# Kernel optimization log

Hardware: AMD Instinct MI355X
Metric: run time of the kernel (lower is better)

The kernel has to match this reference:

```python
import jax, jax.numpy as jnp
import numpy as np

N_NODES = 100000
N_EDGES = 1600000
IN_F, HID_F, OUT_F = 128, 64, 40


def setup_inputs() -> dict:
    key = jax.random.key(0)
    ks = jax.random.split(key, 12)
    features = jax.random.normal(ks[0], (N_NODES, IN_F), jnp.float32)
    src = jax.random.randint(ks[1], (N_EDGES,), 0, N_NODES, jnp.int32)
    dst = jax.random.randint(ks[2], (N_EDGES,), 0, N_NODES, jnp.int32)

    def glorot(k, fi, fo):
        s = np.sqrt(6.0 / (fi + fo)).astype(np.float32)
        return jax.random.uniform(k, (fi, fo), jnp.float32, -s, s)

    return {
        "features": features, "src": src, "dst": dst,
        "W0": glorot(ks[3], IN_F, HID_F), "b0": jnp.zeros((HID_F,), jnp.float32),
        "W1": glorot(ks[4], HID_F, HID_F), "b1": jnp.zeros((HID_F,), jnp.float32),
        "W2": glorot(ks[5], HID_F, HID_F), "b2": jnp.zeros((HID_F,), jnp.float32),
        "W3": glorot(ks[6], HID_F, OUT_F), "b3": jnp.zeros((OUT_F,), jnp.float32),
    }


def _degree_norms(src, dst, n, dtype):
    ones = jnp.ones(src.shape[0], dtype)
    out_deg = jax.ops.segment_sum(ones, src, num_segments=n)
    in_deg = jax.ops.segment_sum(ones, dst, num_segments=n)
    # norm='both': D_src^{-1/2} on sources, D_dst^{-1/2} on destinations (0 for isolated nodes)
    ns = jnp.where(out_deg > 0, jax.lax.rsqrt(jnp.maximum(out_deg, 1.0)), 0.0)[:, None]
    nd = jnp.where(in_deg > 0, jax.lax.rsqrt(jnp.maximum(in_deg, 1.0)), 0.0)[:, None]
    return ns, nd


def _graph_conv(x, W, b, src, dst, ns, nd, relu):
    # transform first (in_feats >= out_feats here), then aggregate: traffic-optimal order
    h = (x * ns) @ W                                   # [N, out_f]
    agg = jax.ops.segment_sum(h[src], dst, num_segments=x.shape[0])  # SpMM gather/scatter
    out = agg * nd + b
    return jax.nn.relu(out) if relu else out


def reference(features, src, dst, W0, b0, W1, b1, W2, b2, W3, b3):
    ns, nd = _degree_norms(src, dst, features.shape[0], features.dtype)
    h = _graph_conv(features, W0, b0, src, dst, ns, nd, True)
    h = _graph_conv(h, W1, b1, src, dst, ns, nd, True)   # dropout = identity (eval)
    h = _graph_conv(h, W2, b2, src, dst, ns, nd, True)
    h = _graph_conv(h, W3, b3, src, dst, ns, nd, False)
    return h
```

## Files before the change

### kernel.cpp

```cpp
#include <hip/hip_runtime.h>
#include <hip/hip_fp16.h>


constexpr int BLK = 256;
constexpr int BIN_SHIFT = 7;
constexpr int BIN_NODES = 128;
constexpr int BIN_CAP = 3072;
constexpr int MAX_NB = 800;
constexpr int EPT = 8;

__global__ void zero_int(int* p, int n) {
  int i = blockIdx.x * blockDim.x + threadIdx.x;
  if (i < n) p[i] = 0;
}

__global__ __launch_bounds__(BLK) void binfill(const int* __restrict__ src,
                                               const int* __restrict__ dst,
                                               int* __restrict__ deg_out,
                                               int* __restrict__ bin_cnt,
                                               int* __restrict__ codes,
                                               int e, int nb) {
  __shared__ int hist[MAX_NB];
  __shared__ int basec[MAX_NB];
  const int tid = threadIdx.x;
  for (int i = tid; i < nb; i += BLK) hist[i] = 0;
  __syncthreads();

  const int B0 = blockIdx.x * (BLK * EPT);
  int s[EPT], d[EPT];
  #pragma unroll
  for (int c = 0; c < EPT / 4; ++c) {
    int i = B0 + (c * BLK + tid) * 4;
    if (i + 3 < e) {
      int4 sv = *(const int4*)(src + i);
      int4 dv = *(const int4*)(dst + i);
      s[4 * c + 0] = sv.x; s[4 * c + 1] = sv.y;
      s[4 * c + 2] = sv.z; s[4 * c + 3] = sv.w;
      d[4 * c + 0] = dv.x; d[4 * c + 1] = dv.y;
      d[4 * c + 2] = dv.z; d[4 * c + 3] = dv.w;
    } else {
      #pragma unroll
      for (int j = 0; j < 4; ++j) {
        int ii = i + j;
        if (ii < e) { s[4 * c + j] = src[ii]; d[4 * c + j] = dst[ii]; }
        else { s[4 * c + j] = 0; d[4 * c + j] = -1; }
      }
    }
  }

  #pragma unroll
  for (int j = 0; j < EPT; ++j) {
    if (d[j] >= 0) {
      atomicAdd(&deg_out[s[j]], 1);
      atomicAdd(&hist[d[j] >> BIN_SHIFT], 1);
    }
  }
  __syncthreads();
  for (int i = tid; i < nb; i += BLK) {
    int c = hist[i];
    basec[i] = c ? atomicAdd(&bin_cnt[i], c) : 0;
  }
  __syncthreads();
  #pragma unroll
  for (int j = 0; j < EPT; ++j) {
    if (d[j] >= 0) {
      int b = d[j] >> BIN_SHIFT;
      int ofs = atomicAdd(&basec[b], 1);
      if (ofs < BIN_CAP)
        codes[(size_t)b * BIN_CAP + ofs] = ((d[j] & (BIN_NODES - 1)) << 17) | s[j];
    }
  }
}

__global__ void norms_ns(const int* __restrict__ deg_out, float* ns, int n) {
  int i = blockIdx.x * blockDim.x + threadIdx.x;
  if (i < n) {
    int od = deg_out[i];
    ns[i] = od > 0 ? rsqrtf((float)od) : 0.f;
  }
}

__global__ __launch_bounds__(BLK) void scan_bins(const int* __restrict__ bin_cnt,
                                                 int* __restrict__ bin_base,
                                                 int* __restrict__ row_ptr,
                                                 int nb, int n) {
  const int tid = threadIdx.x;
  const int base = tid * 4;
  int v0 = 0, v1 = 0, v2 = 0, v3 = 0;
  if (base + 0 < nb) v0 = min(bin_cnt[base + 0], BIN_CAP);
  if (base + 1 < nb) v1 = min(bin_cnt[base + 1], BIN_CAP);
  if (base + 2 < nb) v2 = min(bin_cnt[base + 2], BIN_CAP);
  if (base + 3 < nb) v3 = min(bin_cnt[base + 3], BIN_CAP);
  int s = v0 + v1 + v2 + v3;
  const int lane = tid & 63, wid = tid >> 6;
  int incl = s;
  #pragma unroll
  for (int off = 1; off < 64; off <<= 1) {
    int t = __shfl_up(incl, off, 64);
    if (lane >= off) incl += t;
  }
  __shared__ int wtot[4];
  if (lane == 63) wtot[wid] = incl;
  __syncthreads();
  int woff = 0;
  for (int w = 0; w < wid; ++w) woff += wtot[w];
  int run = woff + (incl - s);
  if (base + 0 < nb) bin_base[base + 0] = run; run += v0;
  if (base + 1 < nb) bin_base[base + 1] = run; run += v1;
  if (base + 2 < nb) bin_base[base + 2] = run; run += v2;
  if (base + 3 < nb) bin_base[base + 3] = run; run += v3;
  if (tid == BLK - 1) {
    int total = wtot[0] + wtot[1] + wtot[2] + wtot[3];
    bin_base[nb] = total;
    row_ptr[n] = total;
  }
}

__global__ __launch_bounds__(BLK) void bin2csr(const int* __restrict__ codes,
                                               const int* __restrict__ bin_cnt,
                                               const int* __restrict__ bin_base,
                                               int* __restrict__ row_ptr,
                                               float* __restrict__ nd,
                                               int* __restrict__ esrc, int n) {
  __shared__ int scodes[BIN_CAP];
  __shared__ int hist[BIN_NODES];
  __shared__ int rowof[BIN_NODES];
  __shared__ int wsum[2];
  const int tid = threadIdx.x;
  const int bin = blockIdx.x;
  const int cnt = min(bin_cnt[bin], BIN_CAP);
  const int base = bin_base[bin];
  const int* cb = codes + (size_t)bin * BIN_CAP;

  if (tid < BIN_NODES) hist[tid] = 0;
  for (int i = tid; i < cnt; i += BLK) scodes[i] = cb[i];
  __syncthreads();
  for (int i = tid; i < cnt; i += BLK) atomicAdd(&hist[scodes[i] >> 17], 1);
  __syncthreads();

  if (tid < BIN_NODES) {
    int v = hist[tid];
    int incl = v;
    const int lane = tid & 63, wid = tid >> 6;
    #pragma unroll
    for (int off = 1; off < 64; off <<= 1) {
      int t = __shfl_up(incl, off, 64);
      if (lane >= off) incl += t;
    }
    if (lane == 63) wsum[wid] = incl;
    __syncthreads();
    int excl = incl - v + (wid ? wsum[0] : 0);
    rowof[tid] = excl;
    int node = bin * BIN_NODES + tid;
    if (node < n) {
      row_ptr[node] = base + excl;
      nd[node] = v > 0 ? rsqrtf((float)v) : 0.f;
    }
  } else {
    __syncthreads();
  }
  __syncthreads();

  for (int i = tid; i < cnt; i += BLK) {
    int code = scodes[i];
    int pos = atomicAdd(&rowof[code >> 17], 1);
    esrc[base + pos] = code & 0x1FFFF;
  }
}

template <int K, int F, int STRIDE>
__global__ __launch_bounds__(BLK) void gemm_tile(const float* __restrict__ x,
                                                 const float* __restrict__ W,
                                                 const float* __restrict__ ns,
                                                 __half* __restrict__ h, int n) {
  constexpr int KT = 64;
  constexpr int KP = KT + 4;
  __shared__ float sx[64 * KP];
  __shared__ float sW[KT * F];
  const int tid = threadIdx.x;
  const int n0 = blockIdx.x * 64;
  const int ft = tid & 15, nt = tid >> 4;
  const int fbase = (4 * ft < F) ? 4 * ft : 0;
  float acc[4][4] = {};

  for (int kt = 0; kt < K; kt += KT) {
    if (kt) __syncthreads();
    for (int i = tid; i < KT * F; i += BLK) sW[i] = W[kt * F + i];
    for (int idx = tid; idx < 64 * (KT / 4); idx += BLK) {
      int node = idx >> 4;
      int kk = idx & 15;
      int gn = min(n0 + node, n - 1);
      float4 v = *(const float4*)(x + (size_t)gn * K + kt + kk * 4);
      *(float4*)(sx + node * KP + kk * 4) = v;
    }
    __syncthreads();

    #pragma unroll 4
    for (int k0 = 0; k0 < KT; k0 += 4) {
      float4 xv0 = *(const float4*)(sx + (4 * nt + 0) * KP + k0);
      float4 xv1 = *(const float4*)(sx + (4 * nt + 1) * KP + k0);
      float4 xv2 = *(const float4*)(sx + (4 * nt + 2) * KP + k0);
      float4 xv3 = *(const float4*)(sx + (4 * nt + 3) * KP + k0);
      float4 w0 = *(const float4*)(sW + (k0 + 0) * F + fbase);
      float4 w1 = *(const float4*)(sW + (k0 + 1) * F + fbase);
      float4 w2 = *(const float4*)(sW + (k0 + 2) * F + fbase);
      float4 w3 = *(const float4*)(sW + (k0 + 3) * F + fbase);
#define GCN_STEP(C, WV)                                                  \
      acc[0][0] = fmaf(xv0.C, WV.x, acc[0][0]);                          \
      acc[0][1] = fmaf(xv0.C, WV.y, acc[0][1]);                          \
      acc[0][2] = fmaf(xv0.C, WV.z, acc[0][2]);                          \
      acc[0][3] = fmaf(xv0.C, WV.w, acc[0][3]);                          \
      acc[1][0] = fmaf(xv1.C, WV.x, acc[1][0]);                          \
      acc[1][1] = fmaf(xv1.C, WV.y, acc[1][1]);                          \
      acc[1][2] = fmaf(xv1.C, WV.z, acc[1][2]);                          \
      acc[1][3] = fmaf(xv1.C, WV.w, acc[1][3]);                          \
      acc[2][0] = fmaf(xv2.C, WV.x, acc[2][0]);                          \
      acc[2][1] = fmaf(xv2.C, WV.y, acc[2][1]);                          \
      acc[2][2] = fmaf(xv2.C, WV.z, acc[2][2]);                          \
      acc[2][3] = fmaf(xv2.C, WV.w, acc[2][3]);                          \
      acc[3][0] = fmaf(xv3.C, WV.x, acc[3][0]);                          \
      acc[3][1] = fmaf(xv3.C, WV.y, acc[3][1]);                          \
      acc[3][2] = fmaf(xv3.C, WV.z, acc[3][2]);                          \
      acc[3][3] = fmaf(xv3.C, WV.w, acc[3][3]);
      GCN_STEP(x, w0)
      GCN_STEP(y, w1)
      GCN_STEP(z, w2)
      GCN_STEP(w, w3)
#undef GCN_STEP
    }
  }

  #pragma unroll
  for (int i = 0; i < 4; ++i) {
    int node = n0 + 4 * nt + i;
    if (node < n && 4 * ft < F) {
      float s = ns[node];
      __half2 h0 = __floats2half2_rn(acc[i][0] * s, acc[i][1] * s);
      __half2 h1 = __floats2half2_rn(acc[i][2] * s, acc[i][3] * s);
      uint2 u;
      u.x = *(unsigned int*)&h0;
      u.y = *(unsigned int*)&h1;
      *(uint2*)(h + (size_t)node * STRIDE + 4 * ft) = u;
    }
  }
}

template <bool RELU>
__global__ void agg4h(const __half* __restrict__ h, const int* __restrict__ row_ptr,
                      const int* __restrict__ esrc, const float* __restrict__ nd,
                      const float* __restrict__ b, float* __restrict__ out, int n) {
  int tid = threadIdx.x;
  int node = blockIdx.x * 4 + (tid >> 6);
  if (node >= n) return;
  int lane = tid & 63;
  int g = lane >> 4;
  int fl = lane & 15;
  int beg = row_ptr[node], end = row_ptr[node + 1];
  float ax = 0.f, ay = 0.f, az = 0.f, aw = 0.f;
  #pragma unroll 4
  for (int k = beg + g; k < end; k += 4) {
    int s = esrc[k];
    uint2 u = *(const uint2*)(h + (size_t)s * 64 + fl * 4);
    float2 f0 = __half22float2(*(__half2*)&u.x);
    float2 f1 = __half22float2(*(__half2*)&u.y);
    ax += f0.x; ay += f0.y; az += f1.x; aw += f1.y;
  }
  ax += __shfl_xor(ax, 16, 64); ay += __shfl_xor(ay, 16, 64);
  az += __shfl_xor(az, 16, 64); aw += __shfl_xor(aw, 16, 64);
  ax += __shfl_xor(ax, 32, 64); ay += __shfl_xor(ay, 32, 64);
  az += __shfl_xor(az, 32, 64); aw += __shfl_xor(aw, 32, 64);
  if (lane < 16) {
    float ndv = nd[node];
    float4 bv = ((const float4*)b)[fl];
    float4 o;
    o.x = ax * ndv + bv.x;
    o.y = ay * ndv + bv.y;
    o.z = az * ndv + bv.z;
    o.w = aw * ndv + bv.w;
    if (RELU) {
      o.x = fmaxf(o.x, 0.f); o.y = fmaxf(o.y, 0.f);
      o.z = fmaxf(o.z, 0.f); o.w = fmaxf(o.w, 0.f);
    }
    *(float4*)(out + (size_t)node * 64 + fl * 4) = o;
  }
}

__global__ void agg40h(const __half* __restrict__ h, const int* __restrict__ row_ptr,
                       const int* __restrict__ esrc, const float* __restrict__ nd,
                       const float* __restrict__ b, float* __restrict__ out, int n) {
  int tid = threadIdx.x;
  int node = blockIdx.x * 4 + (tid >> 6);
  if (node >= n) return;
  int lane = tid & 63;
  int g = lane >> 4;
  int fl = lane & 15;
  int beg = row_ptr[node], end = row_ptr[node + 1];
  float ax = 0.f, ay = 0.f, az = 0.f, aw = 0.f;
  if (fl < 10) {
    #pragma unroll 4
    for (int k = beg + g; k < end; k += 4) {
      int s = esrc[k];
      uint2 u = *(const uint2*)(h + (size_t)s * 40 + fl * 4);
      float2 f0 = __half22float2(*(__half2*)&u.x);
      float2 f1 = __half22float2(*(__half2*)&u.y);
      ax += f0.x; ay += f0.y; az += f1.x; aw += f1.y;
    }
  }
  ax += __shfl_xor(ax, 16, 64); ay += __shfl_xor(ay, 16, 64);
  az += __shfl_xor(az, 16, 64); aw += __shfl_xor(aw, 16, 64);
  ax += __shfl_xor(ax, 32, 64); ay += __shfl_xor(ay, 32, 64);
  az += __shfl_xor(az, 32, 64); aw += __shfl_xor(aw, 32, 64);
  if (lane < 10) {
    float ndv = nd[node];
    float4 bv = ((const float4*)b)[fl];
    float4 o;
    o.x = ax * ndv + bv.x;
    o.y = ay * ndv + bv.y;
    o.z = az * ndv + bv.z;
    o.w = aw * ndv + bv.w;
    *(float4*)(out + (size_t)node * 40 + fl * 4) = o;
  }
}

extern "C" void kernel_launch(void* const* d_in, const int* in_sizes, int n_in,
                              void* d_out, int out_size, void* d_ws, size_t ws_size,
                              hipStream_t stream) {
  const float* features = (const float*)d_in[0];
  const int* src = (const int*)d_in[1];
  const int* dst = (const int*)d_in[2];
  const float* W0 = (const float*)d_in[3];
  const float* b0 = (const float*)d_in[4];
  const float* W1 = (const float*)d_in[5];
  const float* b1 = (const float*)d_in[6];
  const float* W2 = (const float*)d_in[7];
  const float* b2 = (const float*)d_in[8];
  const float* W3 = (const float*)d_in[9];
  const float* b3 = (const float*)d_in[10];

  const int n = in_sizes[0] / 128;
  const int e = in_sizes[1];
  const int nb = (n + BIN_NODES - 1) >> BIN_SHIFT;

  char* p = (char*)d_ws;
  auto alloc = [&](size_t bytes) {
    void* q = (void*)p;
    p += (bytes + 255) & ~(size_t)255;
    return q;
  };
  int* deg_out = (int*)alloc((size_t)(n + nb) * 4);
  int* bin_cnt = deg_out + n;
  float* ns = (float*)alloc((size_t)n * 4);
  float* nd = (float*)alloc((size_t)n * 4);
  int* bin_base = (int*)alloc((size_t)(nb + 1) * 4);
  int* row_ptr = (int*)alloc((size_t)(n + 1) * 4);
  int* codes = (int*)alloc((size_t)nb * BIN_CAP * 4);
  int* esrc = (int*)alloc((size_t)e * 4);
  __half* h = (__half*)alloc((size_t)n * 64 * 2);
  float* xb = (float*)alloc((size_t)n * 64 * 4);

  zero_int<<<(n + nb + BLK - 1) / BLK, BLK, 0, stream>>>(deg_out, n + nb);
  binfill<<<(e + BLK * EPT - 1) / (BLK * EPT), BLK, 0, stream>>>(
      src, dst, deg_out, bin_cnt, codes, e, nb);
  norms_ns<<<(n + BLK - 1) / BLK, BLK, 0, stream>>>(deg_out, ns, n);
  scan_bins<<<1, BLK, 0, stream>>>(bin_cnt, bin_base, row_ptr, nb, n);
  bin2csr<<<nb, BLK, 0, stream>>>(codes, bin_cnt, bin_base, row_ptr, nd, esrc, n);

  const int gnode = (n + 3) / 4;
  const int gblk = (n + 63) / 64;

  gemm_tile<128, 64, 64><<<gblk, BLK, 0, stream>>>(features, W0, ns, h, n);
  agg4h<true><<<gnode, BLK, 0, stream>>>(h, row_ptr, esrc, nd, b0, xb, n);
  gemm_tile<64, 64, 64><<<gblk, BLK, 0, stream>>>(xb, W1, ns, h, n);
  agg4h<true><<<gnode, BLK, 0, stream>>>(h, row_ptr, esrc, nd, b1, xb, n);
  gemm_tile<64, 64, 64><<<gblk, BLK, 0, stream>>>(xb, W2, ns, h, n);
  agg4h<true><<<gnode, BLK, 0, stream>>>(h, row_ptr, esrc, nd, b2, xb, n);
  gemm_tile<64, 40, 40><<<gblk, BLK, 0, stream>>>(xb, W3, ns, h, n);
  agg40h<<<gnode, BLK, 0, stream>>>(h, row_ptr, esrc, nd, b3, (float*)d_out, n);
}
```

Baseline: 398.5 us.

## Bin source edges for out-degree counting and add 8-edge-parallel aggregation

Out-degrees are no longer computed with global atomics on random source nodes. Source edges are now binned in the same fill pass, and a per-bin shared-memory histogram kernel turns them into the source norms. EPT is doubled to 16, and layers 0 and 2 switch to a new aggregation kernel that processes 8 edges in parallel with 16-byte loads per lane. The cost is writing an extra codes array and more register and shared-memory pressure in the fill kernel. Layers 1 and 2 now use different aggregation kernels, which suggests the new one is being A/B tested.

```diff
diff --git a/kernel.cpp b/kernel.cpp
--- a/kernel.cpp
+++ b/kernel.cpp
@@ -7,23 +7,26 @@
 constexpr int BIN_NODES = 128;
 constexpr int BIN_CAP = 3072;
 constexpr int MAX_NB = 800;
-constexpr int EPT = 8;
+constexpr int EPT = 16;
 
 __global__ void zero_int(int* p, int n) {
   int i = blockIdx.x * blockDim.x + threadIdx.x;
   if (i < n) p[i] = 0;
 }
 
-__global__ __launch_bounds__(BLK) void binfill(const int* __restrict__ src,
-                                               const int* __restrict__ dst,
-                                               int* __restrict__ deg_out,
-                                               int* __restrict__ bin_cnt,
-                                               int* __restrict__ codes,
-                                               int e, int nb) {
-  __shared__ int hist[MAX_NB];
-  __shared__ int basec[MAX_NB];
+__global__ __launch_bounds__(BLK) void binfill2(const int* __restrict__ src,
+                                                const int* __restrict__ dst,
+                                                int* __restrict__ bin_cnt_d,
+                                                int* __restrict__ bin_cnt_s,
+                                                int* __restrict__ codes_d,
+                                                int* __restrict__ codes_s,
+                                                int e, int nb) {
+  __shared__ int hist_d[MAX_NB];
+  __shared__ int hist_s[MAX_NB];
+  __shared__ int base_d[MAX_NB];
+  __shared__ int base_s[MAX_NB];
   const int tid = threadIdx.x;
-  for (int i = tid; i < nb; i += BLK) hist[i] = 0;
+  for (int i = tid; i < nb; i += BLK) { hist_d[i] = 0; hist_s[i] = 0; }
   __syncthreads();
 
   const int B0 = blockIdx.x * (BLK * EPT);
@@ -51,32 +54,51 @@
   #pragma unroll
   for (int j = 0; j < EPT; ++j) {
     if (d[j] >= 0) {
-      atomicAdd(&deg_out[s[j]], 1);
-      atomicAdd(&hist[d[j] >> BIN_SHIFT], 1);
+      atomicAdd(&hist_d[d[j] >> BIN_SHIFT], 1);
+      atomicAdd(&hist_s[s[j] >> BIN_SHIFT], 1);
     }
   }
   __syncthreads();
   for (int i = tid; i < nb; i += BLK) {
-    int c = hist[i];
-    basec[i] = c ? atomicAdd(&bin_cnt[i], c) : 0;
+    int cd = hist_d[i];
+    base_d[i] = cd ? atomicAdd(&bin_cnt_d[i], cd) : 0;
+    int cs = hist_s[i];
+    base_s[i] = cs ? atomicAdd(&bin_cnt_s[i], cs) : 0;
   }
   __syncthreads();
   #pragma unroll
   for (int j = 0; j < EPT; ++j) {
     if (d[j] >= 0) {
-      int b = d[j] >> BIN_SHIFT;
-      int ofs = atomicAdd(&basec[b], 1);
-      if (ofs < BIN_CAP)
-        codes[(size_t)b * BIN_CAP + ofs] = ((d[j] & (BIN_NODES - 1)) << 17) | s[j];
-    }
-  }
-}
-
-__global__ void norms_ns(const int* __restrict__ deg_out, float* ns, int n) {
-  int i = blockIdx.x * blockDim.x + threadIdx.x;
-  if (i < n) {
-    int od = deg_out[i];
-    ns[i] = od > 0 ? rsqrtf((float)od) : 0.f;
+      int bd = d[j] >> BIN_SHIFT;
+      int od = atomicAdd(&base_d[bd], 1);
+      if (od < BIN_CAP)
+        codes_d[(size_t)bd * BIN_CAP + od] = ((d[j] & (BIN_NODES - 1)) << 17) | s[j];
+      int bs = s[j] >> BIN_SHIFT;
+      int os = atomicAdd(&base_s[bs], 1);
+      if (os < BIN_CAP)
+        codes_s[(size_t)bs * BIN_CAP + os] = s[j] & (BIN_NODES - 1);
+    }
+  }
+}
+
+__global__ __launch_bounds__(BLK) void bin2deg(const int* __restrict__ codes_s,
+                                               const int* __restrict__ bin_cnt_s,
+                                               float* __restrict__ ns, int n) {
+  __shared__ int hist[BIN_NODES];
+  const int tid = threadIdx.x;
+  if (tid < BIN_NODES) hist[tid] = 0;
+  __syncthreads();
+  const int bin = blockIdx.x;
+  const int cnt = min(bin_cnt_s[bin], BIN_CAP);
+  const int* cb = codes_s + (size_t)bin * BIN_CAP;
+  for (int i = tid; i < cnt; i += BLK) atomicAdd(&hist[cb[i]], 1);
+  __syncthreads();
+  if (tid < BIN_NODES) {
+    int node = bin * BIN_NODES + tid;
+    if (node < n) {
+      int v = hist[tid];
+      ns[node] = v > 0 ? rsqrtf((float)v) : 0.f;
+    }
   }
 }
 
@@ -285,6 +307,57 @@
   }
 }
 
+template <bool RELU>
+__global__ void agg8h(const __half* __restrict__ h, const int* __restrict__ row_ptr,
+                      const int* __restrict__ esrc, const float* __restrict__ nd,
+                      const float* __restrict__ b, float* __restrict__ out, int n) {
+  int tid = threadIdx.x;
+  int node = blockIdx.x * 4 + (tid >> 6);
+  if (node >= n) return;
+  int lane = tid & 63;
+  int g = lane >> 3;
+  int fl = lane & 7;
+  int beg = row_ptr[node], end = row_ptr[node + 1];
+  float4 A0 = {0.f, 0.f, 0.f, 0.f}, A1 = {0.f, 0.f, 0.f, 0.f};
+  #pragma unroll 2
+  for (int k = beg + g; k < end; k += 8) {
+    int s = esrc[k];
+    uint4 u = *(const uint4*)(h + (size_t)s * 64 + fl * 8);
+    float2 f0 = __half22float2(*(__half2*)&u.x);
+    float2 f1 = __half22float2(*(__half2*)&u.y);
+    float2 f2 = __half22float2(*(__half2*)&u.z);
+    float2 f3 = __half22float2(*(__half2*)&u.w);
+    A0.x += f0.x; A0.y += f0.y; A0.z += f1.x; A0.w += f1.y;
+    A1.x += f2.x; A1.y += f2.y; A1.z += f3.x; A1.w += f3.y;
+  }
+  #pragma unroll
+  for (int off = 8; off < 64; off <<= 1) {
+    A0.x += __shfl_xor(A0.x, off, 64); A0.y += __shfl_xor(A0.y, off, 64);
+    A0.z += __shfl_xor(A0.z, off, 64); A0.w += __shfl_xor(A0.w, off, 64);
+    A1.x += __shfl_xor(A1.x, off, 64); A1.y += __shfl_xor(A1.y, off, 64);
+    A1.z += __shfl_xor(A1.z, off, 64); A1.w += __shfl_xor(A1.w, off, 64);
+  }
+  if (lane < 8) {
+    float ndv = nd[node];
+    float4 b0 = ((const float4*)b)[2 * fl];
+    float4 b1 = ((const float4*)b)[2 * fl + 1];
+    float4 o0, o1;
+    o0.x = A0.x * ndv + b0.x; o0.y = A0.y * ndv + b0.y;
+    o0.z = A0.z * ndv + b0.z; o0.w = A0.w * ndv + b0.w;
+    o1.x = A1.x * ndv + b1.x; o1.y = A1.y * ndv + b1.y;
+    o1.z = A1.z * ndv + b1.z; o1.w = A1.w * ndv + b1.w;
+    if (RELU) {
+      o0.x = fmaxf(o0.x, 0.f); o0.y = fmaxf(o0.y, 0.f);
+      o0.z = fmaxf(o0.z, 0.f); o0.w = fmaxf(o0.w, 0.f);
+      o1.x = fmaxf(o1.x, 0.f); o1.y = fmaxf(o1.y, 0.f);
+      o1.z = fmaxf(o1.z, 0.f); o1.w = fmaxf(o1.w, 0.f);
+    }
+    float* op = out + (size_t)node * 64 + fl * 8;
+    *(float4*)(op) = o0;
+    *(float4*)(op + 4) = o1;
+  }
+}
+
 __global__ void agg40h(const __half* __restrict__ h, const int* __restrict__ row_ptr,
                        const int* __restrict__ esrc, const float* __restrict__ nd,
                        const float* __restrict__ b, float* __restrict__ out, int n) {
@@ -347,33 +420,34 @@
     p += (bytes + 255) & ~(size_t)255;
     return q;
   };
-  int* deg_out = (int*)alloc((size_t)(n + nb) * 4);
-  int* bin_cnt = deg_out + n;
+  int* bin_cnt_d = (int*)alloc((size_t)2 * nb * 4);
+  int* bin_cnt_s = bin_cnt_d + nb;
   float* ns = (float*)alloc((size_t)n * 4);
   float* nd = (float*)alloc((size_t)n * 4);
   int* bin_base = (int*)alloc((size_t)(nb + 1) * 4);
   int* row_ptr = (int*)alloc((size_t)(n + 1) * 4);
-  int* codes = (int*)alloc((size_t)nb * BIN_CAP * 4);
+  int* codes_d = (int*)alloc((size_t)nb * BIN_CAP * 4);
+  int* codes_s = (int*)alloc((size_t)nb * BIN_CAP * 4);
   int* esrc = (int*)alloc((size_t)e * 4);
   __half* h = (__half*)alloc((size_t)n * 64 * 2);
   float* xb = (float*)alloc((size_t)n * 64 * 4);
 
-  zero_int<<<(n + nb + BLK - 1) / BLK, BLK, 0, stream>>>(deg_out, n + nb);
-  binfill<<<(e + BLK * EPT - 1) / (BLK * EPT), BLK, 0, stream>>>(
-      src, dst, deg_out, bin_cnt, codes, e, nb);
-  norms_ns<<<(n + BLK - 1) / BLK, BLK, 0, stream>>>(deg_out, ns, n);
-  scan_bins<<<1, BLK, 0, stream>>>(bin_cnt, bin_base, row_ptr, nb, n);
-  bin2csr<<<nb, BLK, 0, stream>>>(codes, bin_cnt, bin_base, row_ptr, nd, esrc, n);
+  zero_int<<<(2 * nb + BLK - 1) / BLK, BLK, 0, stream>>>(bin_cnt_d, 2 * nb);
+  binfill2<<<(e + BLK * EPT - 1) / (BLK * EPT), BLK, 0, stream>>>(
+      src, dst, bin_cnt_d, bin_cnt_s, codes_d, codes_s, e, nb);
+  bin2deg<<<nb, BLK, 0, stream>>>(codes_s, bin_cnt_s, ns, n);
+  scan_bins<<<1, BLK, 0, stream>>>(bin_cnt_d, bin_base, row_ptr, nb, n);
+  bin2csr<<<nb, BLK, 0, stream>>>(codes_d, bin_cnt_d, bin_base, row_ptr, nd, esrc, n);
 
   const int gnode = (n + 3) / 4;
   const int gblk = (n + 63) / 64;
 
   gemm_tile<128, 64, 64><<<gblk, BLK, 0, stream>>>(features, W0, ns, h, n);
-  agg4h<true><<<gnode, BLK, 0, stream>>>(h, row_ptr, esrc, nd, b0, xb, n);
+  agg8h<true><<<gnode, BLK, 0, stream>>>(h, row_ptr, esrc, nd, b0, xb, n);
   gemm_tile<64, 64, 64><<<gblk, BLK, 0, stream>>>(xb, W1, ns, h, n);
   agg4h<true><<<gnode, BLK, 0, stream>>>(h, row_ptr, esrc, nd, b1, xb, n);
   gemm_tile<64, 64, 64><<<gblk, BLK, 0, stream>>>(xb, W2, ns, h, n);
-  agg4h<true><<<gnode, BLK, 0, stream>>>(h, row_ptr, esrc, nd, b2, xb, n);
+  agg8h<true><<<gnode, BLK, 0, stream>>>(h, row_ptr, esrc, nd, b2, xb, n);
   gemm_tile<64, 40, 40><<<gblk, BLK, 0, stream>>>(xb, W3, ns, h, n);
   agg40h<<<gnode, BLK, 0, stream>>>(h, row_ptr, esrc, nd, b3, (float*)d_out, n);
 }
```

Result: faster. 340.4 us (-14.6%).
